# Kernel tuning notes

Hardware: AMD Instinct MI355X
Metric: run time of the kernel (lower is better)

Reference implementation:

```python
import jax, jax.numpy as jnp
import numpy as np

B, S, T = 32, 400, 64
V, E, H = 32000, 256, 512


def _lstm_step(x, h, c, W_ih, W_hh, b):
    # PyTorch LSTM gate order: i, f, g, o
    g = x @ W_ih.T + h @ W_hh.T + b
    i, f, gg, o = jnp.split(g, 4, axis=-1)
    i = jax.nn.sigmoid(i)
    f = jax.nn.sigmoid(f)
    gg = jnp.tanh(gg)
    o = jax.nn.sigmoid(o)
    c_new = f * c + i * gg
    h_new = o * jnp.tanh(c_new)
    return h_new, c_new


def setup_inputs() -> dict:
    key = jax.random.key(0)
    ks = jax.random.split(key, 32)
    d = {}
    d['src'] = jax.random.randint(ks[0], (B, S), 1, V)
    d['src_lengths'] = jnp.full((B,), S, dtype=jnp.int32)
    d['tgt'] = jax.random.randint(ks[1], (B, T), 1, V)
    sc = 0.05
    emb = jax.random.normal(ks[2], (V, E), jnp.float32) * sc
    d['emb'] = emb.at[0].set(0.0)  # padding_idx=0
    d['enc_W_ih_f'] = jax.random.normal(ks[3], (4 * H, E), jnp.float32) * sc
    d['enc_W_hh_f'] = jax.random.normal(ks[4], (4 * H, H), jnp.float32) * sc
    d['enc_b_ih_f'] = jax.random.normal(ks[5], (4 * H,), jnp.float32) * sc
    d['enc_b_hh_f'] = jax.random.normal(ks[6], (4 * H,), jnp.float32) * sc
    d['enc_W_ih_b'] = jax.random.normal(ks[7], (4 * H, E), jnp.float32) * sc
    d['enc_W_hh_b'] = jax.random.normal(ks[8], (4 * H, H), jnp.float32) * sc
    d['enc_b_ih_b'] = jax.random.normal(ks[9], (4 * H,), jnp.float32) * sc
    d['enc_b_hh_b'] = jax.random.normal(ks[10], (4 * H,), jnp.float32) * sc
    d['enc_init_h'] = jax.random.uniform(ks[11], (2, H), jnp.float32, -0.01, 0.01)
    d['enc_init_c'] = jax.random.uniform(ks[12], (2, H), jnp.float32, -0.01, 0.01)
    d['dec_h_W'] = jax.random.normal(ks[13], (H, 2 * H), jnp.float32) * sc
    d['dec_c_W'] = jax.random.normal(ks[14], (H, 2 * H), jnp.float32) * sc
    d['cell_W_ih'] = jax.random.normal(ks[15], (4 * H, E), jnp.float32) * sc
    d['cell_W_hh'] = jax.random.normal(ks[16], (4 * H, H), jnp.float32) * sc
    d['cell_b_ih'] = jax.random.normal(ks[17], (4 * H,), jnp.float32) * sc
    d['cell_b_hh'] = jax.random.normal(ks[18], (4 * H,), jnp.float32) * sc
    d['attn_W'] = jax.random.normal(ks[19], (H, 2 * H), jnp.float32) * sc
    d['attn_b'] = jax.random.normal(ks[20], (H,), jnp.float32) * sc
    d['concat_W'] = jax.random.normal(ks[21], (H, 3 * H), jnp.float32) * sc
    d['concat_b'] = jax.random.normal(ks[22], (H,), jnp.float32) * sc
    d['out_W'] = jax.random.normal(ks[23], (V, H), jnp.float32) * sc
    d['out_b'] = jax.random.normal(ks[24], (V,), jnp.float32) * sc
    return d


def reference(src, src_lengths, tgt, emb,
              enc_W_ih_f, enc_W_hh_f, enc_b_ih_f, enc_b_hh_f,
              enc_W_ih_b, enc_W_hh_b, enc_b_ih_b, enc_b_hh_b,
              enc_init_h, enc_init_c, dec_h_W, dec_c_W,
              cell_W_ih, cell_W_hh, cell_b_ih, cell_b_hh,
              attn_W, attn_b, concat_W, concat_b, out_W, out_b):
    Bs, Ss = src.shape
    Hs = enc_init_h.shape[1]
    xe = emb[src].transpose(1, 0, 2)  # [S, B, E]

    # ---- bi-LSTM encoder (all lengths == S, so packing is identity) ----
    h0f = jnp.broadcast_to(enc_init_h[0], (Bs, Hs))
    c0f = jnp.broadcast_to(enc_init_c[0], (Bs, Hs))
    h0b = jnp.broadcast_to(enc_init_h[1], (Bs, Hs))
    c0b = jnp.broadcast_to(enc_init_c[1], (Bs, Hs))

    def enc_fwd(carry, x):
        h, c = carry
        h, c = _lstm_step(x, h, c, enc_W_ih_f, enc_W_hh_f, enc_b_ih_f + enc_b_hh_f)
        return (h, c), h

    def enc_bwd(carry, x):
        h, c = carry
        h, c = _lstm_step(x, h, c, enc_W_ih_b, enc_W_hh_b, enc_b_ih_b + enc_b_hh_b)
        return (h, c), h

    (hf, cf), out_f = jax.lax.scan(enc_fwd, (h0f, c0f), xe)
    (hb, cb), out_b_seq = jax.lax.scan(enc_bwd, (h0b, c0b), xe[::-1])
    out_b_seq = out_b_seq[::-1]
    enc_outs = jnp.concatenate([out_f, out_b_seq], axis=-1)  # [S, B, 2H]

    # bridge final states to decoder init
    dec_h = jnp.concatenate([hf, hb], axis=-1) @ dec_h_W.T  # [B, H]
    dec_c = jnp.concatenate([cf, cb], axis=-1) @ dec_c_W.T

    mask = jnp.arange(Ss)[None, :] < src_lengths[:, None]  # [B, S]
    attn_keys = enc_outs @ attn_W.T + attn_b  # [S, B, H]

    def dec_step(carry, t_ids):
        h, c = carry
        x = emb[t_ids]  # [B, E]
        h, c = _lstm_step(x, h, c, cell_W_ih, cell_W_hh, cell_b_ih + cell_b_hh)
        scores = jnp.einsum('bh,sbh->bs', h, attn_keys)
        scores = jnp.where(mask, scores, jnp.float32(-1e18))
        w = jax.nn.softmax(scores, axis=1)  # [B, S]
        context = jnp.einsum('bs,sbd->bd', w, enc_outs)  # [B, 2H]
        cc = jnp.tanh(jnp.concatenate([context, h], axis=-1) @ concat_W.T + concat_b)
        logit = jax.nn.log_softmax(cc @ out_W.T + out_b, axis=-1)  # [B, V]
        return (h, c), logit

    _, logits = jax.lax.scan(dec_step, (dec_h, dec_c), tgt.T)  # [T, B, V]
    return logits.transpose(1, 0, 2)  # [B, T, V]
```

## Files before the change

### kernel.cpp

```cpp
#include <hip/hip_runtime.h>
#include <math.h>

#define BB 32
#define SS 400
#define TT 64
#define VV 32000
#define EE 256
#define HH 512

typedef __attribute__((ext_vector_type(4))) float f32x4;
typedef __attribute__((ext_vector_type(8))) short bf16x8t;
typedef __attribute__((ext_vector_type(8))) unsigned short u16x8;
typedef __attribute__((ext_vector_type(4))) unsigned int u32x4;
typedef unsigned long long u64t;

__device__ __forceinline__ ushort f2bf(float x) {
  uint u = __float_as_uint(x);
  return (ushort)((u + 0x7fffu + ((u >> 16) & 1u)) >> 16);
}
__device__ __forceinline__ float bf2f(ushort x) {
  return __uint_as_float(((uint)x) << 16);
}
__device__ __forceinline__ float fsigmoid(float x) {
  return 1.f / (1.f + __expf(-x));
}
__device__ __forceinline__ float ftanh(float x) {
  return 1.f - 2.f / (__expf(2.f * x) + 1.f);
}
__device__ __forceinline__ void gload_lds16(const ushort* g, ushort* l) {
  __builtin_amdgcn_global_load_lds(
      (const __attribute__((address_space(1))) void*)g,
      (__attribute__((address_space(3))) void*)l, 16, 0, 0);
}
__device__ __forceinline__ void unpack8(uint4 u, float* f) {
  f[0] = __uint_as_float(u.x << 16); f[1] = __uint_as_float(u.x & 0xffff0000u);
  f[2] = __uint_as_float(u.y << 16); f[3] = __uint_as_float(u.y & 0xffff0000u);
  f[4] = __uint_as_float(u.z << 16); f[5] = __uint_as_float(u.z & 0xffff0000u);
  f[6] = __uint_as_float(u.w << 16); f[7] = __uint_as_float(u.w & 0xffff0000u);
}

__global__ __launch_bounds__(256) void init_all_kernel(
    const float* __restrict__ einh, uint* __restrict__ hge,
    uint* __restrict__ hgb)
{
  int i = blockIdx.x * 256 + threadIdx.x;
  if (i < 4096) {
    int c = (i & 127) * 4;
    uint lo = (uint)f2bf(einh[c]) | ((uint)f2bf(einh[c + 1]) << 16);
    uint hi = (uint)f2bf(einh[c + 2]) | ((uint)f2bf(einh[c + 3]) << 16);
    u32x4 pkt = {lo, hi, 0u, 0u};
    *(u32x4*)(hge + (size_t)i * 4) = pkt;
  } else if (i < 8192) {
    int p = i - 4096;
    int c = HH + (p & 127) * 4;
    uint lo = (uint)f2bf(einh[c]) | ((uint)f2bf(einh[c + 1]) << 16);
    uint hi = (uint)f2bf(einh[c + 2]) | ((uint)f2bf(einh[c + 3]) << 16);
    u32x4 pkt = {lo, hi, 0u, 0u};
    *(u32x4*)(hgb + (size_t)p * 4) = pkt;
  }
}

__global__ __launch_bounds__(256) void f2bf_kernel(
    const float* __restrict__ in, ushort* __restrict__ out, long n)
{
  long step = (long)gridDim.x * 256 * 4;
  for (long i = ((long)blockIdx.x * 256 + threadIdx.x) * 4; i < n; i += step) {
    float4 v = *(const float4*)(in + i);
    ushort4 o;
    o.x = f2bf(v.x); o.y = f2bf(v.y); o.z = f2bf(v.z); o.w = f2bf(v.w);
    *(ushort4*)(out + i) = o;
  }
}

__global__ __launch_bounds__(64) void gather_x_kernel(
    const float* __restrict__ emb, const int* __restrict__ tok, int L,
    ushort* __restrict__ xout)
{
  int row = blockIdx.x;
  int b = row & 31, s = row >> 5;
  int t = tok[b * L + s];
  float4 v = ((const float4*)(emb + (size_t)t * EE))[threadIdx.x];
  ushort4 o;
  o.x = f2bf(v.x); o.y = f2bf(v.y); o.z = f2bf(v.z); o.w = f2bf(v.w);
  ((ushort4*)(xout + (size_t)row * EE))[threadIdx.x] = o;
}

__global__ __launch_bounds__(256) void bias3_kernel(
    const float* a1, const float* a2, const float* b1, const float* b2,
    const float* c1, const float* c2, float* out)
{
  int i = blockIdx.x * 256 + threadIdx.x;
  if (i < 2048) out[i] = a1[i] + a2[i];
  else if (i < 4096) out[i] = b1[i - 2048] + b2[i - 2048];
  else if (i < 6144) out[i] = c1[i - 4096] + c2[i - 4096];
}

__global__ __launch_bounds__(256) void gemm_mfma_kernel(
    const ushort* __restrict__ A, const ushort* __restrict__ B,
    const float* __restrict__ bias, void* __restrict__ Cout,
    int M, int N, int K, int flags)
{
  __shared__ ushort Asub[128 * 32], Bsub[128 * 32];
  int tid = threadIdx.x;
  int w = tid >> 6, l = tid & 63;
  int n0 = blockIdx.x * 128, m0 = blockIdx.y * 128;
  int wm = w >> 1, wn = w & 1;

  int srow = 16 * 2 * w + (l >> 2);
  int scol = (l & 3) * 8;
  const ushort* Ar0 = A + (size_t)(m0 + srow) * K + scol;
  const ushort* Ar1 = Ar0 + (size_t)16 * K;
  const ushort* Br0 = B + (size_t)(n0 + srow) * K + scol;
  const ushort* Br1 = Br0 + (size_t)16 * K;
  ushort* ldsA0 = Asub + (2 * w) * 512;
  ushort* ldsA1 = Asub + (2 * w + 1) * 512;
  ushort* ldsB0 = Bsub + (2 * w) * 512;
  ushort* ldsB1 = Bsub + (2 * w + 1) * 512;

  f32x4 acc[4][4];
  #pragma unroll
  for (int i = 0; i < 4; ++i)
    #pragma unroll
    for (int j = 0; j < 4; ++j)
      acc[i][j] = (f32x4){0.f, 0.f, 0.f, 0.f};

  int lr = l & 15, lkb = (l >> 4) * 8;

  for (int k0 = 0; k0 < K; k0 += 32) {
    gload_lds16(Ar0 + k0, ldsA0);
    gload_lds16(Ar1 + k0, ldsA1);
    gload_lds16(Br0 + k0, ldsB0);
    gload_lds16(Br1 + k0, ldsB1);
    __syncthreads();
    bf16x8t af[4], bfv[4];
    #pragma unroll
    for (int mf = 0; mf < 4; ++mf)
      af[mf] = *(const bf16x8t*)&Asub[(wm * 64 + mf * 16 + lr) * 32 + lkb];
    #pragma unroll
    for (int nf = 0; nf < 4; ++nf)
      bfv[nf] = *(const bf16x8t*)&Bsub[(wn * 64 + nf * 16 + lr) * 32 + lkb];
    #pragma unroll
    for (int mf = 0; mf < 4; ++mf)
      #pragma unroll
      for (int nf = 0; nf < 4; ++nf)
        acc[mf][nf] = __builtin_amdgcn_mfma_f32_16x16x32_bf16(
            af[mf], bfv[nf], acc[mf][nf], 0, 0, 0);
    __syncthreads();
  }

  int lg = l >> 4;
  #pragma unroll
  for (int mf = 0; mf < 4; ++mf) {
    #pragma unroll
    for (int nf = 0; nf < 4; ++nf) {
      int n = n0 + wn * 64 + nf * 16 + lr;
      float bv = bias[n];
      #pragma unroll
      for (int r = 0; r < 4; ++r) {
        int m = m0 + wm * 64 + mf * 16 + lg * 4 + r;
        float v = acc[mf][nf][r] + bv;
        if (flags & 1) v = tanhf(v);
        if (flags & 8) {
          int s = m >> 5, b = m & 31;
          int gate = n >> 9, col = n & 511;
          size_t dst = (((size_t)s * 32 + (col >> 4)) * 32 + b) * 64 +
                       (size_t)(col & 15) * 4 + gate;
          ((ushort*)Cout)[dst] = f2bf(v);
        } else {
          int row = (flags & 2) ? ((m & 31) * TT + (m >> 5)) : m;
          if (flags & 4) ((ushort*)Cout)[(size_t)row * N + n] = f2bf(v);
          else           ((float*)Cout)[(size_t)row * N + n] = v;
        }
      }
    }
  }
}

struct PersistArgs {
  const float* W_hh;
  const ushort* xw;
  uint* hpack;
  const float* c_init_elem;
  const float* c_init_bcast;
  ushort* out_h;
  int out_os, out_ofs;
  int steps, backward;
  float* h_final;
  float* c_final;
};

__global__ __launch_bounds__(256) void lstm_persist_kernel(
    PersistArgs A0, PersistArgs A1, int nblk_dir,
    const float* __restrict__ cvt_in, ushort* __restrict__ cvt_out, long cvt_n)
{
  __shared__ ushort ldsW[64 * 512];
  __shared__ ushort ldsH[32 * 512];
  __shared__ ushort ldsX[32 * 64];

  int bid = (int)blockIdx.x;
  if (bid >= 2 * nblk_dir) {
    int nc = (int)gridDim.x - 2 * nblk_dir;
    long base = ((long)(bid - 2 * nblk_dir) * 256 + threadIdx.x) * 4;
    long step = (long)nc * 256 * 4;
    for (long i = base; i < cvt_n; i += step) {
      float4 v = *(const float4*)(cvt_in + i);
      ushort4 o;
      o.x = f2bf(v.x); o.y = f2bf(v.y); o.z = f2bf(v.z); o.w = f2bf(v.w);
      *(ushort4*)(cvt_out + i) = o;
    }
    return;
  }

  PersistArgs a = (bid < nblk_dir) ? A0 : A1;
  int cblk = bid % nblk_dir;
  int c0 = cblk * 16;
  int tid = threadIdx.x;
  int w = tid >> 6, l = tid & 63;
  int lr = l & 15, kb = (l >> 4) * 8;
  int g = l & 3;
  int col = c0 + w * 4 + (lr >> 2);
  int n = w * 16 + lr;

  {
    int nn = tid >> 2;
    int kbase = (tid & 3) * 128;
    int rW = (nn & 3) * HH + c0 + (nn >> 2);
    const float4* src = (const float4*)(a.W_hh + (size_t)rW * HH + kbase);
    #pragma unroll
    for (int j = 0; j < 16; ++j) {
      float4 u = src[2 * j], v = src[2 * j + 1];
      u16x8 o;
      o[0] = f2bf(u.x); o[1] = f2bf(u.y); o[2] = f2bf(u.z); o[3] = f2bf(u.w);
      o[4] = f2bf(v.x); o[5] = f2bf(v.y); o[6] = f2bf(v.z); o[7] = f2bf(v.w);
      int k = kbase + j * 8;
      int byte = (nn * 1024 + k * 2) ^ ((nn & 7) << 4);
      *(u16x8*)((char*)ldsW + byte) = o;
    }
  }

  float creg[2][4];
  #pragma unroll
  for (int mf = 0; mf < 2; ++mf)
    #pragma unroll
    for (int r = 0; r < 4; ++r) {
      int b = mf * 16 + (l >> 4) * 4 + r;
      creg[mf][r] = a.c_init_bcast ? a.c_init_bcast[col]
                                   : a.c_init_elem[b * HH + col];
    }
  __syncthreads();

  bf16x8t wfr[16];
  {
    int wr = w * 16 + lr;
    #pragma unroll
    for (int kf = 0; kf < 16; ++kf) {
      int ka = kf * 32 + kb;
      wfr[kf] = *(const bf16x8t*)((const char*)ldsW +
                ((wr * 1024 + ka * 2) ^ ((wr & 7) << 4)));
    }
  }

  int prow0 = tid >> 7;
  int pcp4 = tid & 127;

  int s0i = a.backward ? (a.steps - 1) : 0;
  float4 xcur = *(const float4*)(a.xw + ((size_t)s0i * 32 + cblk) * 2048 + tid * 8);
  float4 xnext;

  for (int it = 0; it < a.steps; ++it) {
    int s = a.backward ? (a.steps - 1 - it) : it;
    const uint* hsrc = a.hpack + (size_t)(it & 1) * 4096 * 4;
    uint* hdst = a.hpack + (size_t)((it + 1) & 1) * 4096 * 4;

    u32x4 pv[16];
    #pragma unroll
    for (int j = 0; j < 16; ++j) {
      const uint* ap = hsrc + (size_t)((prow0 + 2 * j) * 128 + pcp4) * 4;
      asm volatile("global_load_dwordx4 %0, %1, off sc0 sc1"
                   : "=&v"(pv[j]) : "v"(ap) : "memory");
    }
    asm volatile("s_waitcnt vmcnt(0)" ::: "memory");
    __builtin_amdgcn_sched_barrier(0);
    {
      int guard = 0;
      while (true) {
        uint bad = 0;
        #pragma unroll
        for (int j = 0; j < 16; ++j) bad |= (pv[j][2] ^ (uint)it);
        if (bad == 0) break;
        if (++guard > (1 << 18)) break;
        __builtin_amdgcn_s_sleep(1);
        #pragma unroll
        for (int j = 0; j < 16; ++j) {
          const uint* ap = hsrc + (size_t)((prow0 + 2 * j) * 128 + pcp4) * 4;
          asm volatile("global_load_dwordx4 %0, %1, off sc0 sc1"
                       : "=&v"(pv[j]) : "v"(ap) : "memory");
        }
        asm volatile("s_waitcnt vmcnt(0)" ::: "memory");
        __builtin_amdgcn_sched_barrier(0);
      }
    }
    __syncthreads();

    #pragma unroll
    for (int j = 0; j < 16; ++j) {
      int row = prow0 + 2 * j;
      int byte = (row * 1024 + pcp4 * 8) ^ ((row & 7) << 4);
      *(u64t*)((char*)ldsH + byte) = ((u64t)pv[j][1] << 32) | (u64t)pv[j][0];
    }
    *(float4*)&ldsX[tid * 8] = xcur;
    __syncthreads();

    f32x4 acc0 = (f32x4){0.f, 0.f, 0.f, 0.f};
    f32x4 acc1 = (f32x4){0.f, 0.f, 0.f, 0.f};
    #pragma unroll
    for (int kf = 0; kf < 16; ++kf) {
      int ka = kf * 32 + kb;
      bf16x8t av0 = *(const bf16x8t*)((const char*)ldsH + ((lr * 1024 + ka * 2) ^ ((lr & 7) << 4)));
      bf16x8t av1 = *(const bf16x8t*)((const char*)ldsH + (((16 + lr) * 1024 + ka * 2) ^ (((16 + lr) & 7) << 4)));
      acc0 = __builtin_amdgcn_mfma_f32_16x16x32_bf16(av0, wfr[kf], acc0, 0, 0, 0);
      acc1 = __builtin_amdgcn_mfma_f32_16x16x32_bf16(av1, wfr[kf], acc1, 0, 0, 0);
    }

    u64t pk[2][4];
    #pragma unroll
    for (int mf = 0; mf < 2; ++mf) {
      f32x4 ac = mf ? acc1 : acc0;
      #pragma unroll
      for (int r = 0; r < 4; ++r) {
        int b = mf * 16 + (l >> 4) * 4 + r;
        float v = ac[r] + bf2f(ldsX[b * 64 + n]);
        float av = (g == 2) ? ftanh(v) : fsigmoid(v);
        float a1 = __shfl_xor(av, 1);
        float a2 = __shfl_xor(av, 2);
        float a3 = __shfl_xor(av, 3);
        float hnew = 0.f;
        if (g == 0) {
          float iv = av, fv = a1, gv = a2, ov = a3;
          float cnew = fv * creg[mf][r] + iv * gv;
          hnew = ov * ftanh(cnew);
          creg[mf][r] = cnew;
          if (a.h_final && it == a.steps - 1) {
            a.h_final[b * HH + col] = hnew;
            a.c_final[b * HH + col] = cnew;
          }
        }
        uint hu = (uint)f2bf(hnew);
        uint p1 = __shfl_xor(hu, 4);
        uint p2 = __shfl_xor(hu, 8);
        uint p3 = __shfl_xor(p1, 8);
        uint lo = hu | (p1 << 16);
        uint hi = p2 | (p3 << 16);
        pk[mf][r] = ((u64t)hi << 32) | (u64t)lo;
      }
    }

    if ((l & 15) == 0 && it + 1 < a.steps) {
      int cp4w = cblk * 4 + w;
      #pragma unroll
      for (int mf = 0; mf < 2; ++mf)
        #pragma unroll
        for (int r = 0; r < 4; ++r) {
          int b = mf * 16 + (l >> 4) * 4 + r;
          u32x4 pkt;
          pkt[0] = (uint)pk[mf][r];
          pkt[1] = (uint)(pk[mf][r] >> 32);
          pkt[2] = (uint)(it + 1);
          pkt[3] = 0u;
          uint* dp = hdst + (size_t)(b * 128 + cp4w) * 4;
          asm volatile("global_store_dwordx4 %0, %1, off sc0 sc1"
                       :: "v"(dp), "v"(pkt) : "memory");
        }
    }

    if ((l & 15) == 0) {
      #pragma unroll
      for (int mf = 0; mf < 2; ++mf)
        #pragma unroll
        for (int r = 0; r < 4; ++r) {
          int b = mf * 16 + (l >> 4) * 4 + r;
          *(u64t*)(a.out_h + (size_t)s * BB * a.out_os + b * a.out_os +
                   a.out_ofs + c0 + w * 4) = pk[mf][r];
        }
    }
    if (it + 1 < a.steps) {
      int sn = a.backward ? (a.steps - 2 - it) : (it + 1);
      const ushort* xp = a.xw + ((size_t)sn * 32 + cblk) * 2048 + tid * 8;
      asm volatile("global_load_dwordx4 %0, %1, off"
                   : "=&v"(xnext) : "v"(xp) : "memory");
    }
    xcur = xnext;
  }
}

__global__ __launch_bounds__(256) void dec_init_kernel(
    const float* __restrict__ hf, const float* __restrict__ hb,
    const float* __restrict__ cf, const float* __restrict__ cb,
    const float* __restrict__ Wh, const float* __restrict__ Wc,
    uint* __restrict__ dh_pack, float* __restrict__ dc)
{
  int b = blockIdx.x;
  __shared__ float hcat[2 * HH], ccat[2 * HH];
  __shared__ ushort dhs[HH];
  int tid = threadIdx.x;
  for (int i = tid; i < HH; i += 256) {
    hcat[i] = hf[b * HH + i]; hcat[HH + i] = hb[b * HH + i];
    ccat[i] = cf[b * HH + i]; ccat[HH + i] = cb[b * HH + i];
  }
  __syncthreads();
  for (int col = tid; col < HH; col += 256) {
    const float4* wh = (const float4*)(Wh + (size_t)col * (2 * HH));
    const float4* wc = (const float4*)(Wc + (size_t)col * (2 * HH));
    float ah = 0.f, acv = 0.f;
    #pragma unroll 4
    for (int k4 = 0; k4 < (2 * HH) / 4; ++k4) {
      float4 h4 = *(const float4*)&hcat[k4 * 4];
      float4 w4 = wh[k4];
      ah += h4.x * w4.x + h4.y * w4.y + h4.z * w4.z + h4.w * w4.w;
      float4 c4 = *(const float4*)&ccat[k4 * 4];
      float4 v4 = wc[k4];
      acv += c4.x * v4.x + c4.y * v4.y + c4.z * v4.z + c4.w * v4.w;
    }
    dhs[col] = f2bf(ah);
    dc[b * HH + col] = acv;
  }
  __syncthreads();
  if (tid < 128) {
    int c = tid * 4;
    uint lo = (uint)dhs[c] | ((uint)dhs[c + 1] << 16);
    uint hi = (uint)dhs[c + 2] | ((uint)dhs[c + 3] << 16);
    u32x4 pkt = {lo, hi, 0u, 0u};
    *(u32x4*)(dh_pack + (size_t)(b * 128 + tid) * 4) = pkt;
  }
}

__global__ __launch_bounds__(256) void scores_kernel(
    const ushort* __restrict__ keys_bf, const ushort* __restrict__ dhall,
    const int* __restrict__ slen, float* __restrict__ sc)
{
  int b = blockIdx.x & 31, s0 = ((int)blockIdx.x >> 5) * 16;
  __shared__ ushort ldsD[64][520];
  __shared__ ushort ldsK[16][520];
  int tid = threadIdx.x;
  #pragma unroll
  for (int j = 0; j < 16; ++j) {
    int ci = tid + 256 * j;
    int row = ci >> 6, c8 = (ci & 63) * 8;
    *(u16x8*)&ldsD[row][c8] = *(const u16x8*)(dhall + ((size_t)row * BB + b) * HH + c8);
  }
  #pragma unroll
  for (int j = 0; j < 4; ++j) {
    int ci = tid + 256 * j;
    int row = ci >> 6, c8 = (ci & 63) * 8;
    *(u16x8*)&ldsK[row][c8] = *(const u16x8*)(keys_bf + ((size_t)(s0 + row) * BB + b) * HH + c8);
  }
  __syncthreads();

  int sl = tid & 15, tq = tid >> 4;
  float acc[4] = {0.f, 0.f, 0.f, 0.f};
  for (int k8 = 0; k8 < 64; ++k8) {
    float kv[8];
    unpack8(*(const uint4*)&ldsK[sl][k8 * 8], kv);
    #pragma unroll
    for (int j = 0; j < 4; ++j) {
      float dv[8];
      unpack8(*(const uint4*)&ldsD[tq * 4 + j][k8 * 8], dv);
      #pragma unroll
      for (int e = 0; e < 8; ++e) acc[j] += kv[e] * dv[e];
    }
  }
  int s = s0 + sl;
  int len = slen[b];
  #pragma unroll
  for (int j = 0; j < 4; ++j) {
    int t = tq * 4 + j;
    sc[((size_t)t * BB + b) * SS + s] = (s < len) ? acc[j] : -1e18f;
  }
}

__global__ __launch_bounds__(64) void softmax_kernel(
    const float* __restrict__ sc, ushort* __restrict__ wbf)
{
  int row = blockIdx.x;
  int tid = threadIdx.x;
  float v[7];
  float m = -3e38f;
  #pragma unroll
  for (int j = 0; j < 7; ++j) {
    int s = tid + 64 * j;
    v[j] = (s < SS) ? sc[(size_t)row * SS + s] : -3e38f;
    m = fmaxf(m, v[j]);
  }
  #pragma unroll
  for (int o = 32; o; o >>= 1) m = fmaxf(m, __shfl_xor(m, o));
  float ssum = 0.f;
  float p[7];
  #pragma unroll
  for (int j = 0; j < 7; ++j) {
    int s = tid + 64 * j;
    p[j] = (s < SS) ? __expf(v[j] - m) : 0.f;
    ssum += p[j];
  }
  #pragma unroll
  for (int o = 32; o; o >>= 1) ssum += __shfl_xor(ssum, o);
  float inv = 1.f / ssum;
  #pragma unroll
  for (int j = 0; j < 7; ++j) {
    int s = tid + 64 * j;
    if (s < 416) wbf[(size_t)row * 416 + s] = (s < SS) ? f2bf(p[j] * inv) : (ushort)0;
  }
}

__global__ __launch_bounds__(256) void context_kernel(
    const ushort* __restrict__ wbf, const ushort* __restrict__ enc,
    const ushort* __restrict__ dhall, ushort* __restrict__ catb)
{
  int b = blockIdx.x, ch = blockIdx.y;
  int tid = threadIdx.x;
  if (ch >= 16) {
    int c0 = (ch - 16) * 64;
    #pragma unroll
    for (int j = 0; j < 2; ++j) {
      int ci = tid + 256 * j;
      int t = ci >> 3, u = ci & 7;
      *(u16x8*)(catb + ((size_t)t * BB + b) * 1536 + 1024 + c0 + u * 8) =
          *(const u16x8*)(dhall + ((size_t)t * BB + b) * HH + c0 + u * 8);
    }
    return;
  }
  int d0 = ch * 64;
  __shared__ ushort ldsWt[64][424];
  for (int ci = tid; ci < 64 * 52; ci += 256) {
    int t = ci / 52, u = ci % 52;
    *(u16x8*)&ldsWt[t][u * 8] = *(const u16x8*)(wbf + (size_t)(t * BB + b) * 416 + u * 8);
  }
  __syncthreads();

  int d = d0 + (tid & 63), tq = tid >> 6;
  float acc16[16];
  #pragma unroll
  for (int i = 0; i < 16; ++i) acc16[i] = 0.f;

  for (int s8 = 0; s8 < 50; ++s8) {
    float ev[8];
    #pragma unroll
    for (int e = 0; e < 8; ++e)
      ev[e] = bf2f(enc[((size_t)(s8 * 8 + e) * BB + b) * 1024 + d]);
    #pragma unroll
    for (int i = 0; i < 16; ++i) {
      float wv[8];
      unpack8(*(const uint4*)&ldsWt[tq * 16 + i][s8 * 8], wv);
      #pragma unroll
      for (int e = 0; e < 8; ++e) acc16[i] += wv[e] * ev[e];
    }
  }
  #pragma unroll
  for (int i = 0; i < 16; ++i) {
    int t = tq * 16 + i;
    catb[((size_t)t * BB + b) * 1536 + d] = f2bf(acc16[i]);
  }
}

__global__ __launch_bounds__(1024) void logsoftmax_kernel(float* __restrict__ out)
{
  int r = blockIdx.x;
  __shared__ float row[VV];
  __shared__ float red[16];
  int tid = threadIdx.x;
  float4* p = (float4*)(out + (size_t)r * VV);
  float4* rp = (float4*)row;
  float m = -3e38f;
  #pragma unroll
  for (int j = 0; j < 8; ++j) {
    int i = tid + 1024 * j;
    if (i < VV / 4) {
      float4 v = p[i];
      rp[i] = v;
      m = fmaxf(m, fmaxf(fmaxf(v.x, v.y), fmaxf(v.z, v.w)));
    }
  }
  #pragma unroll
  for (int o = 32; o; o >>= 1) m = fmaxf(m, __shfl_xor(m, o));
  if ((tid & 63) == 0) red[tid >> 6] = m;
  __syncthreads();
  float mm = red[0];
  #pragma unroll
  for (int i = 1; i < 16; ++i) mm = fmaxf(mm, red[i]);
  __syncthreads();
  float ssum = 0.f;
  #pragma unroll
  for (int j = 0; j < 8; ++j) {
    int i = tid + 1024 * j;
    if (i < VV / 4) {
      float4 v = rp[i];
      ssum += __expf(v.x - mm) + __expf(v.y - mm) + __expf(v.z - mm) + __expf(v.w - mm);
    }
  }
  #pragma unroll
  for (int o = 32; o; o >>= 1) ssum += __shfl_xor(ssum, o);
  if ((tid & 63) == 0) red[tid >> 6] = ssum;
  __syncthreads();
  float st = red[0];
  #pragma unroll
  for (int i = 1; i < 16; ++i) st += red[i];
  st = mm + logf(st);
  #pragma unroll
  for (int j = 0; j < 8; ++j) {
    int i = tid + 1024 * j;
    if (i < VV / 4) {
      float4 v = rp[i];
      v.x -= st; v.y -= st; v.z -= st; v.w -= st;
      p[i] = v;
    }
  }
}

extern "C" void kernel_launch(void* const* d_in, const int* in_sizes, int n_in,
                              void* d_out, int out_size, void* d_ws, size_t ws_size,
                              hipStream_t stream)
{
  (void)in_sizes; (void)n_in; (void)out_size; (void)ws_size;
  const int*   src  = (const int*)d_in[0];
  const int*   slen = (const int*)d_in[1];
  const int*   tgt  = (const int*)d_in[2];
  const float* emb  = (const float*)d_in[3];
  const float* eWif = (const float*)d_in[4];
  const float* eWhf = (const float*)d_in[5];
  const float* ebif = (const float*)d_in[6];
  const float* ebhf = (const float*)d_in[7];
  const float* eWib = (const float*)d_in[8];
  const float* eWhb = (const float*)d_in[9];
  const float* ebib = (const float*)d_in[10];
  const float* ebhb = (const float*)d_in[11];
  const float* einh = (const float*)d_in[12];
  const float* einc = (const float*)d_in[13];
  const float* dhW  = (const float*)d_in[14];
  const float* dcW  = (const float*)d_in[15];
  const float* cWi  = (const float*)d_in[16];
  const float* cWh  = (const float*)d_in[17];
  const float* cbi  = (const float*)d_in[18];
  const float* cbh  = (const float*)d_in[19];
  const float* aW   = (const float*)d_in[20];
  const float* abv  = (const float*)d_in[21];
  const float* ccW  = (const float*)d_in[22];
  const float* ccbv = (const float*)d_in[23];
  const float* oW   = (const float*)d_in[24];
  const float* obv  = (const float*)d_in[25];
  float* out = (float*)d_out;
  float* ws  = (float*)d_ws;

  size_t off = 0;
  ushort* enc_bf  = (ushort*)(ws + off); off += (size_t)SS * BB * 1024 / 2;
  ushort* keys_bf = (ushort*)(ws + off); off += (size_t)SS * BB * HH / 2;
  ushort* dhall_bf= (ushort*)(ws + off); off += (size_t)TT * BB * HH / 2;
  ushort* catb_bf = (ushort*)(ws + off); off += (size_t)TT * BB * 1536 / 2;
  ushort* ccv_bf  = (ushort*)(ws + off); off += (size_t)TT * BB * HH / 2;
  float*  scbuf   = ws + off;            off += (size_t)TT * BB * SS;
  ushort* w_bf    = (ushort*)(ws + off); off += (size_t)TT * BB * 416 / 2;
  ushort* xe_bf   = (ushort*)(ws + off); off += (size_t)SS * BB * EE / 2;
  ushort* xd_bf   = (ushort*)(ws + off); off += (size_t)TT * BB * EE / 2;
  ushort* xWf_bf  = (ushort*)(ws + off); off += (size_t)SS * BB * 2048 / 2;
  ushort* xWb_bf  = (ushort*)(ws + off); off += (size_t)SS * BB * 2048 / 2;
  ushort* xWd_bf  = (ushort*)(ws + off); off += (size_t)TT * BB * 2048 / 2;
  ushort* oW_bf   = (ushort*)(ws + off); off += (size_t)VV * HH / 2;
  ushort* aW_bf   = (ushort*)(ws + off); off += (size_t)HH * 1024 / 2;
  ushort* ccW_bf  = (ushort*)(ws + off); off += (size_t)HH * 1536 / 2;
  ushort* eWif_bf = (ushort*)(ws + off); off += (size_t)2048 * EE / 2;
  ushort* eWib_bf = (ushort*)(ws + off); off += (size_t)2048 * EE / 2;
  ushort* cWi_bf  = (ushort*)(ws + off); off += (size_t)2048 * EE / 2;
  uint* hge_pack = (uint*)(ws + off); off += (size_t)2 * 4096 * 4;
  uint* hgb_pack = (uint*)(ws + off); off += (size_t)2 * 4096 * 4;
  uint* hdec_pack= (uint*)(ws + off); off += (size_t)2 * 4096 * 4;
  float* bias3 = ws + off; off += 3 * 2048;
  float* hf_f  = ws + off; off += BB * HH;
  float* hb_f  = ws + off; off += BB * HH;
  float* cf_f  = ws + off; off += BB * HH;
  float* cb_f  = ws + off; off += BB * HH;
  float* dcb   = ws + off; off += BB * HH;

  hipMemsetAsync(hge_pack, 0, (size_t)3 * 2 * 4096 * 16, stream);

  init_all_kernel<<<64, 256, 0, stream>>>(einh, hge_pack, hgb_pack);

  f2bf_kernel<<<512, 256, 0, stream>>>(aW, aW_bf, (long)HH * 1024);
  f2bf_kernel<<<512, 256, 0, stream>>>(ccW, ccW_bf, (long)HH * 1536);
  f2bf_kernel<<<512, 256, 0, stream>>>(eWif, eWif_bf, (long)2048 * EE);
  f2bf_kernel<<<512, 256, 0, stream>>>(eWib, eWib_bf, (long)2048 * EE);
  f2bf_kernel<<<512, 256, 0, stream>>>(cWi, cWi_bf, (long)2048 * EE);
  bias3_kernel<<<24, 256, 0, stream>>>(ebif, ebhf, ebib, ebhb, cbi, cbh, bias3);

  gather_x_kernel<<<SS * BB, 64, 0, stream>>>(emb, src, SS, xe_bf);
  gather_x_kernel<<<TT * BB, 64, 0, stream>>>(emb, tgt, TT, xd_bf);
  gemm_mfma_kernel<<<dim3(2048 / 128, (SS * BB) / 128), 256, 0, stream>>>(
      xe_bf, eWif_bf, bias3, xWf_bf, SS * BB, 2048, EE, 8);
  gemm_mfma_kernel<<<dim3(2048 / 128, (SS * BB) / 128), 256, 0, stream>>>(
      xe_bf, eWib_bf, bias3 + 2048, xWb_bf, SS * BB, 2048, EE, 8);
  gemm_mfma_kernel<<<dim3(2048 / 128, (TT * BB) / 128), 256, 0, stream>>>(
      xd_bf, cWi_bf, bias3 + 4096, xWd_bf, TT * BB, 2048, EE, 8);

  {
    PersistArgs af, ab;
    af.W_hh = eWhf; af.xw = xWf_bf; af.hpack = hge_pack;
    af.c_init_elem = nullptr; af.c_init_bcast = einc;
    af.out_h = enc_bf; af.out_os = 1024; af.out_ofs = 0;
    af.steps = SS; af.backward = 0;
    af.h_final = hf_f; af.c_final = cf_f;
    ab = af;
    ab.W_hh = eWhb; ab.xw = xWb_bf; ab.hpack = hgb_pack;
    ab.c_init_bcast = einc + HH;
    ab.out_ofs = HH; ab.backward = 1;
    ab.h_final = hb_f; ab.c_final = cb_f;
    lstm_persist_kernel<<<256, 256, 0, stream>>>(af, ab, 32,
                                                 oW, oW_bf, (long)VV * HH);
  }

  dec_init_kernel<<<BB, 256, 0, stream>>>(hf_f, hb_f, cf_f, cb_f, dhW, dcW,
                                          hdec_pack, dcb);
  {
    PersistArgs ad;
    ad.W_hh = cWh; ad.xw = xWd_bf; ad.hpack = hdec_pack;
    ad.c_init_elem = dcb; ad.c_init_bcast = nullptr;
    ad.out_h = dhall_bf; ad.out_os = HH; ad.out_ofs = 0;
    ad.steps = TT; ad.backward = 0;
    ad.h_final = nullptr; ad.c_final = nullptr;
    lstm_persist_kernel<<<32, 256, 0, stream>>>(ad, ad, 32,
                                                nullptr, nullptr, 0);
  }

  gemm_mfma_kernel<<<dim3(HH / 128, (SS * BB) / 128), 256, 0, stream>>>(
      enc_bf, aW_bf, abv, keys_bf, SS * BB, HH, 1024, 4);

  scores_kernel<<<32 * 25, 256, 0, stream>>>(keys_bf, dhall_bf, slen, scbuf);
  softmax_kernel<<<TT * BB, 64, 0, stream>>>(scbuf, w_bf);
  context_kernel<<<dim3(BB, 24), 256, 0, stream>>>(w_bf, enc_bf, dhall_bf, catb_bf);

  gemm_mfma_kernel<<<dim3(HH / 128, (TT * BB) / 128), 256, 0, stream>>>(
      catb_bf, ccW_bf, ccbv, ccv_bf, TT * BB, HH, 1536, 1 | 4);
  gemm_mfma_kernel<<<dim3(VV / 128, (TT * BB) / 128), 256, 0, stream>>>(
      ccv_bf, oW_bf, obv, out, TT * BB, VV, HH, 2);

  logsoftmax_kernel<<<TT * BB, 1024, 0, stream>>>(out);
}
```

Before: 2.966 ms.

## Halve LSTM persistent block count with 512-thread blocks and prepacked bf16 W_hh

The persistent LSTM recurrence kernel now uses 512-thread blocks that each own 32 hidden columns, so 16 blocks per direction replace 32. This changes the xW layout, the LDS x buffer and the h-pack indexing to match. W_hh is converted to bf16 once by a separate kernel and loaded straight into registers, which removes the per-block fp32-to-bf16 conversion staged through LDS. Fewer blocks should cut the per-step cross-block spin-wait on h, but each block does twice the work per step and fewer CUs are busy. The converter tail blocks that fill the remaining grid also shrink.

```diff
diff --git a/kernel.cpp b/kernel.cpp
--- a/kernel.cpp
+++ b/kernel.cpp
@@ -72,6 +72,30 @@
   }
 }
 
+__global__ __launch_bounds__(256) void cvt3_kernel(
+    const float* in0, ushort* out0, long n0,
+    const float* in1, ushort* out1, long n1,
+    const float* in2, ushort* out2, long n2)
+{
+  long base = ((long)blockIdx.x * 256 + threadIdx.x) * 4;
+  long step = (long)gridDim.x * 256 * 4;
+  for (long i = base; i < n0; i += step) {
+    float4 v = *(const float4*)(in0 + i);
+    ushort4 o; o.x = f2bf(v.x); o.y = f2bf(v.y); o.z = f2bf(v.z); o.w = f2bf(v.w);
+    *(ushort4*)(out0 + i) = o;
+  }
+  for (long i = base; i < n1; i += step) {
+    float4 v = *(const float4*)(in1 + i);
+    ushort4 o; o.x = f2bf(v.x); o.y = f2bf(v.y); o.z = f2bf(v.z); o.w = f2bf(v.w);
+    *(ushort4*)(out1 + i) = o;
+  }
+  for (long i = base; i < n2; i += step) {
+    float4 v = *(const float4*)(in2 + i);
+    ushort4 o; o.x = f2bf(v.x); o.y = f2bf(v.y); o.z = f2bf(v.z); o.w = f2bf(v.w);
+    *(ushort4*)(out2 + i) = o;
+  }
+}
+
 __global__ __launch_bounds__(64) void gather_x_kernel(
     const float* __restrict__ emb, const int* __restrict__ tok, int L,
     ushort* __restrict__ xout)
@@ -163,8 +187,8 @@
         if (flags & 8) {
           int s = m >> 5, b = m & 31;
           int gate = n >> 9, col = n & 511;
-          size_t dst = (((size_t)s * 32 + (col >> 4)) * 32 + b) * 64 +
-                       (size_t)(col & 15) * 4 + gate;
+          size_t dst = (((size_t)s * 16 + (col >> 5)) * 32 + b) * 128 +
+                       (size_t)(col & 31) * 4 + gate;
           ((ushort*)Cout)[dst] = f2bf(v);
         } else {
           int row = (flags & 2) ? ((m & 31) * TT + (m >> 5)) : m;
@@ -177,7 +201,7 @@
 }
 
 struct PersistArgs {
-  const float* W_hh;
+  const ushort* W_bf;
   const ushort* xw;
   uint* hpack;
   const float* c_init_elem;
@@ -189,19 +213,19 @@
   float* c_final;
 };
 
-__global__ __launch_bounds__(256) void lstm_persist_kernel(
+__global__ __launch_bounds__(512) void lstm_persist_kernel(
     PersistArgs A0, PersistArgs A1, int nblk_dir,
     const float* __restrict__ cvt_in, ushort* __restrict__ cvt_out, long cvt_n)
 {
-  __shared__ ushort ldsW[64 * 512];
   __shared__ ushort ldsH[32 * 512];
-  __shared__ ushort ldsX[32 * 64];
+  __shared__ ushort ldsX[32 * 128];
 
   int bid = (int)blockIdx.x;
+  int tid = threadIdx.x;
   if (bid >= 2 * nblk_dir) {
     int nc = (int)gridDim.x - 2 * nblk_dir;
-    long base = ((long)(bid - 2 * nblk_dir) * 256 + threadIdx.x) * 4;
-    long step = (long)nc * 256 * 4;
+    long base = ((long)(bid - 2 * nblk_dir) * 512 + tid) * 4;
+    long step = (long)nc * 512 * 4;
     for (long i = base; i < cvt_n; i += step) {
       float4 v = *(const float4*)(cvt_in + i);
       ushort4 o;
@@ -213,30 +237,18 @@
 
   PersistArgs a = (bid < nblk_dir) ? A0 : A1;
   int cblk = bid % nblk_dir;
-  int c0 = cblk * 16;
-  int tid = threadIdx.x;
+  int c0 = cblk * 32;
   int w = tid >> 6, l = tid & 63;
   int lr = l & 15, kb = (l >> 4) * 8;
   int g = l & 3;
-  int col = c0 + w * 4 + (lr >> 2);
   int n = w * 16 + lr;
-
-  {
-    int nn = tid >> 2;
-    int kbase = (tid & 3) * 128;
-    int rW = (nn & 3) * HH + c0 + (nn >> 2);
-    const float4* src = (const float4*)(a.W_hh + (size_t)rW * HH + kbase);
-    #pragma unroll
-    for (int j = 0; j < 16; ++j) {
-      float4 u = src[2 * j], v = src[2 * j + 1];
-      u16x8 o;
-      o[0] = f2bf(u.x); o[1] = f2bf(u.y); o[2] = f2bf(u.z); o[3] = f2bf(u.w);
-      o[4] = f2bf(v.x); o[5] = f2bf(v.y); o[6] = f2bf(v.z); o[7] = f2bf(v.w);
-      int k = kbase + j * 8;
-      int byte = (nn * 1024 + k * 2) ^ ((nn & 7) << 4);
-      *(u16x8*)((char*)ldsW + byte) = o;
-    }
-  }
+  int col = c0 + (n >> 2);
+  const ushort* wrow = a.W_bf + (size_t)((n & 3) * HH + col) * HH + kb;
+
+  bf16x8t wfr[16];
+  #pragma unroll
+  for (int kf = 0; kf < 16; ++kf)
+    wfr[kf] = *(const bf16x8t*)(wrow + kf * 32);
 
   float creg[2][4];
   #pragma unroll
@@ -247,24 +259,12 @@
       creg[mf][r] = a.c_init_bcast ? a.c_init_bcast[col]
                                    : a.c_init_elem[b * HH + col];
     }
-  __syncthreads();
-
-  bf16x8t wfr[16];
-  {
-    int wr = w * 16 + lr;
-    #pragma unroll
-    for (int kf = 0; kf < 16; ++kf) {
-      int ka = kf * 32 + kb;
-      wfr[kf] = *(const bf16x8t*)((const char*)ldsW +
-                ((wr * 1024 + ka * 2) ^ ((wr & 7) << 4)));
-    }
-  }
 
   int prow0 = tid >> 7;
   int pcp4 = tid & 127;
 
   int s0i = a.backward ? (a.steps - 1) : 0;
-  float4 xcur = *(const float4*)(a.xw + ((size_t)s0i * 32 + cblk) * 2048 + tid * 8);
+  float4 xcur = *(const float4*)(a.xw + ((size_t)s0i * 16 + cblk) * 4096 + tid * 8);
   float4 xnext;
 
   for (int it = 0; it < a.steps; ++it) {
@@ -272,10 +272,10 @@
     const uint* hsrc = a.hpack + (size_t)(it & 1) * 4096 * 4;
     uint* hdst = a.hpack + (size_t)((it + 1) & 1) * 4096 * 4;
 
-    u32x4 pv[16];
-    #pragma unroll
-    for (int j = 0; j < 16; ++j) {
-      const uint* ap = hsrc + (size_t)((prow0 + 2 * j) * 128 + pcp4) * 4;
+    u32x4 pv[8];
+    #pragma unroll
+    for (int j = 0; j < 8; ++j) {
+      const uint* ap = hsrc + (size_t)((prow0 + 4 * j) * 128 + pcp4) * 4;
       asm volatile("global_load_dwordx4 %0, %1, off sc0 sc1"
                    : "=&v"(pv[j]) : "v"(ap) : "memory");
     }
@@ -286,13 +286,13 @@
       while (true) {
         uint bad = 0;
         #pragma unroll
-        for (int j = 0; j < 16; ++j) bad |= (pv[j][2] ^ (uint)it);
+        for (int j = 0; j < 8; ++j) bad |= (pv[j][2] ^ (uint)it);
         if (bad == 0) break;
         if (++guard > (1 << 18)) break;
         __builtin_amdgcn_s_sleep(1);
         #pragma unroll
-        for (int j = 0; j < 16; ++j) {
-          const uint* ap = hsrc + (size_t)((prow0 + 2 * j) * 128 + pcp4) * 4;
+        for (int j = 0; j < 8; ++j) {
+          const uint* ap = hsrc + (size_t)((prow0 + 4 * j) * 128 + pcp4) * 4;
           asm volatile("global_load_dwordx4 %0, %1, off sc0 sc1"
                        : "=&v"(pv[j]) : "v"(ap) : "memory");
         }
@@ -303,8 +303,8 @@
     __syncthreads();
 
     #pragma unroll
-    for (int j = 0; j < 16; ++j) {
-      int row = prow0 + 2 * j;
+    for (int j = 0; j < 8; ++j) {
+      int row = prow0 + 4 * j;
       int byte = (row * 1024 + pcp4 * 8) ^ ((row & 7) << 4);
       *(u64t*)((char*)ldsH + byte) = ((u64t)pv[j][1] << 32) | (u64t)pv[j][0];
     }
@@ -329,7 +329,7 @@
       #pragma unroll
       for (int r = 0; r < 4; ++r) {
         int b = mf * 16 + (l >> 4) * 4 + r;
-        float v = ac[r] + bf2f(ldsX[b * 64 + n]);
+        float v = ac[r] + bf2f(ldsX[b * 128 + n]);
         float av = (g == 2) ? ftanh(v) : fsigmoid(v);
         float a1 = __shfl_xor(av, 1);
         float a2 = __shfl_xor(av, 2);
@@ -356,7 +356,7 @@
     }
 
     if ((l & 15) == 0 && it + 1 < a.steps) {
-      int cp4w = cblk * 4 + w;
+      int cp4w = cblk * 8 + w;
       #pragma unroll
       for (int mf = 0; mf < 2; ++mf)
         #pragma unroll
@@ -385,7 +385,7 @@
     }
     if (it + 1 < a.steps) {
       int sn = a.backward ? (a.steps - 2 - it) : (it + 1);
-      const ushort* xp = a.xw + ((size_t)sn * 32 + cblk) * 2048 + tid * 8;
+      const ushort* xp = a.xw + ((size_t)sn * 16 + cblk) * 4096 + tid * 8;
       asm volatile("global_load_dwordx4 %0, %1, off"
                    : "=&v"(xnext) : "v"(xp) : "memory");
     }
@@ -668,6 +668,9 @@
   ushort* eWif_bf = (ushort*)(ws + off); off += (size_t)2048 * EE / 2;
   ushort* eWib_bf = (ushort*)(ws + off); off += (size_t)2048 * EE / 2;
   ushort* cWi_bf  = (ushort*)(ws + off); off += (size_t)2048 * EE / 2;
+  ushort* eWhf_bf = (ushort*)(ws + off); off += (size_t)2048 * HH / 2;
+  ushort* eWhb_bf = (ushort*)(ws + off); off += (size_t)2048 * HH / 2;
+  ushort* cWh_bf  = (ushort*)(ws + off); off += (size_t)2048 * HH / 2;
   uint* hge_pack = (uint*)(ws + off); off += (size_t)2 * 4096 * 4;
   uint* hgb_pack = (uint*)(ws + off); off += (size_t)2 * 4096 * 4;
   uint* hdec_pack= (uint*)(ws + off); off += (size_t)2 * 4096 * 4;
@@ -687,6 +690,9 @@
   f2bf_kernel<<<512, 256, 0, stream>>>(eWif, eWif_bf, (long)2048 * EE);
   f2bf_kernel<<<512, 256, 0, stream>>>(eWib, eWib_bf, (long)2048 * EE);
   f2bf_kernel<<<512, 256, 0, stream>>>(cWi, cWi_bf, (long)2048 * EE);
+  cvt3_kernel<<<512, 256, 0, stream>>>(eWhf, eWhf_bf, (long)2048 * HH,
+                                       eWhb, eWhb_bf, (long)2048 * HH,
+                                       cWh,  cWh_bf,  (long)2048 * HH);
   bias3_kernel<<<24, 256, 0, stream>>>(ebif, ebhf, ebib, ebhb, cbi, cbh, bias3);
 
   gather_x_kernel<<<SS * BB, 64, 0, stream>>>(emb, src, SS, xe_bf);
@@ -700,17 +706,17 @@
 
   {
     PersistArgs af, ab;
-    af.W_hh = eWhf; af.xw = xWf_bf; af.hpack = hge_pack;
+    af.W_bf = eWhf_bf; af.xw = xWf_bf; af.hpack = hge_pack;
     af.c_init_elem = nullptr; af.c_init_bcast = einc;
     af.out_h = enc_bf; af.out_os = 1024; af.out_ofs = 0;
     af.steps = SS; af.backward = 0;
     af.h_final = hf_f; af.c_final = cf_f;
     ab = af;
-    ab.W_hh = eWhb; ab.xw = xWb_bf; ab.hpack = hgb_pack;
+    ab.W_bf = eWhb_bf; ab.xw = xWb_bf; ab.hpack = hgb_pack;
     ab.c_init_bcast = einc + HH;
     ab.out_ofs = HH; ab.backward = 1;
     ab.h_final = hb_f; ab.c_final = cb_f;
-    lstm_persist_kernel<<<256, 256, 0, stream>>>(af, ab, 32,
+    lstm_persist_kernel<<<128, 512, 0, stream>>>(af, ab, 16,
                                                  oW, oW_bf, (long)VV * HH);
   }
 
@@ -718,12 +724,12 @@
                                           hdec_pack, dcb);
   {
     PersistArgs ad;
-    ad.W_hh = cWh; ad.xw = xWd_bf; ad.hpack = hdec_pack;
+    ad.W_bf = cWh_bf; ad.xw = xWd_bf; ad.hpack = hdec_pack;
     ad.c_init_elem = dcb; ad.c_init_bcast = nullptr;
     ad.out_h = dhall_bf; ad.out_os = HH; ad.out_ofs = 0;
     ad.steps = TT; ad.backward = 0;
     ad.h_final = nullptr; ad.c_final = nullptr;
-    lstm_persist_kernel<<<32, 256, 0, stream>>>(ad, ad, 32,
+    lstm_persist_kernel<<<16, 512, 0, stream>>>(ad, ad, 16,
                                                 nullptr, nullptr, 0);
   }
 
```

Result: slower. 4.527 ms (+52.6%).
